# Performance work log

Hardware: AMD Instinct MI355X
Metric: run time of the kernel (lower is better)

Reference implementation:

```python
import jax, jax.numpy as jnp
import numpy as np

N = 50000      # nodes
E = 800000     # edges (avg degree 16)
D = 128        # in_dim
H = 128        # hidden_dim
C = 10         # num_classes
G = 128        # graphs in batch
NUM_LAYERS = 3


def setup_inputs() -> dict:
    key = jax.random.key(0)
    ks = jax.random.split(key, 32)
    inp = {
        'features': jax.random.normal(ks[0], (N, D), dtype=jnp.float32),
        'src': jax.random.randint(ks[1], (E,), 0, N, dtype=jnp.int32),
        'dst': jax.random.randint(ks[2], (E,), 0, N, dtype=jnp.int32),
        'graph_ids': jnp.sort(jax.random.randint(ks[3], (N,), 0, G, dtype=jnp.int32)),
        'eps': jnp.zeros((NUM_LAYERS,), dtype=jnp.float32),  # learn_eps=True, init 0
    }
    # GIN MLPs: layer i has linear1 [in,H], linear2 [H,H] (stored as [in,out])
    ki = 4
    for i in range(NUM_LAYERS):
        din = D if i == 0 else H
        inp[f'w1_{i}'] = jax.random.normal(ks[ki], (din, H), dtype=jnp.float32) * (1.0 / np.sqrt(din)); ki += 1
        inp[f'b1_{i}'] = jnp.zeros((H,), dtype=jnp.float32)
        inp[f'w2_{i}'] = jax.random.normal(ks[ki], (H, H), dtype=jnp.float32) * (1.0 / np.sqrt(H)); ki += 1
        inp[f'b2_{i}'] = jnp.zeros((H,), dtype=jnp.float32)
    inp['wc1'] = jax.random.normal(ks[ki], (H, H), dtype=jnp.float32) * (1.0 / np.sqrt(H)); ki += 1
    inp['bc1'] = jnp.zeros((H,), dtype=jnp.float32)
    inp['wc2'] = jax.random.normal(ks[ki], (H, C), dtype=jnp.float32) * (1.0 / np.sqrt(H)); ki += 1
    inp['bc2'] = jnp.zeros((C,), dtype=jnp.float32)
    return inp


def _mlp(x, w1, b1, w2, b2):
    return jax.nn.relu(x @ w1 + b1) @ w2 + b2


def reference(features, src, dst, graph_ids, eps,
              w1_0, b1_0, w2_0, b2_0,
              w1_1, b1_1, w2_1, b2_1,
              w1_2, b1_2, w2_2, b2_2,
              wc1, bc1, wc2, bc2):
    mlps = [(w1_0, b1_0, w2_0, b2_0), (w1_1, b1_1, w2_1, b2_1), (w1_2, b1_2, w2_2, b2_2)]
    h = features
    for i, (w1, b1, w2, b2) in enumerate(mlps):
        # GINConv: aggregate sum of in-neighbor features (gather src, segment-sum into dst)
        agg = jax.ops.segment_sum(h[src], dst, num_segments=N)
        h = (1.0 + eps[i]) * h + agg
        h = _mlp(h, w1, b1, w2, b2)
        h = jax.nn.relu(h)
    # SumPooling: nodes -> graphs
    hg = jax.ops.segment_sum(h, graph_ids, num_segments=G)  # [G, H]
    out = jax.nn.relu(hg @ wc1 + bc1) @ wc2 + bc2            # [G, C]
    return out
```

## Files before the change

kernel.cpp:

```cpp
#include <hip/hip_runtime.h>

#define NN 50000
#define EE 800000
#define HH 128
#define CC 10
#define GG 128
#define NBK 782
#define NCH 98
#define CHUNK 8192

typedef __attribute__((ext_vector_type(8))) short short8;
typedef __attribute__((ext_vector_type(4))) float f32x4;

__device__ __forceinline__ ushort f2b(float f) {
    union { float f; uint u; } x; x.f = f;
    uint u = x.u;
    uint r = (u + 0x7fffu + ((u >> 16) & 1u)) >> 16;
    return (ushort)r;
}
__device__ __forceinline__ float lo2f(uint v) {
    union { uint u; float f; } x; x.u = v << 16; return x.f;
}
__device__ __forceinline__ float hi2f(uint v) {
    union { uint u; float f; } x; x.u = v & 0xffff0000u; return x.f;
}


__global__ __launch_bounds__(256) void prep_kernel(const float* __restrict__ features,
                                                   const float* w0, const float* w1,
                                                   const float* w2, const float* w3,
                                                   const float* w4, const float* w5,
                                                   const int* __restrict__ dst,
                                                   ushort* __restrict__ hb0,
                                                   ushort* __restrict__ wt,
                                                   int* __restrict__ hist,
                                                   float* __restrict__ hg,
                                                   int* __restrict__ counter) {
    __shared__ int hc[NBK];
    const int b = blockIdx.x, t = threadIdx.x;
    if (b < 6250) {
        int idx = b * 256 + t;
        float4 v = *(const float4*)(features + (size_t)idx * 4);
        ushort4 o;
        o.x = f2b(v.x); o.y = f2b(v.y); o.z = f2b(v.z); o.w = f2b(v.w);
        *(ushort4*)(hb0 + (size_t)idx * 4) = o;
    } else if (b < 6634) {
        int idx = (b - 6250) * 256 + t;
        int mi = idx >> 14, rest = idx & 16383;
        int n = rest >> 7, k = rest & 127;
        const float* src;
        switch (mi) {
            case 0: src = w0; break; case 1: src = w1; break;
            case 2: src = w2; break; case 3: src = w3; break;
            case 4: src = w4; break; default: src = w5; break;
        }
        wt[mi * 16384 + n * 128 + k] = f2b(src[k * 128 + n]);
    } else if (b < 6732) {
        const int c = b - 6634;
        for (int k = t; k < NBK; k += 256) hc[k] = 0;
        __syncthreads();
        for (int j = 0; j < 32; ++j) {
            int e = c * CHUNK + j * 256 + t;
            if (e < EE) atomicAdd(&hc[dst[e] >> 6], 1);
        }
        __syncthreads();
        for (int k = t; k < NBK; k += 256) hist[k * NCH + c] = hc[k];
    } else {
        int idx = (b - 6732) * 256 + t;
        hg[idx] = 0.f;
        if (b == 6732 && t == 0) *counter = 0;
    }
}

__global__ __launch_bounds__(128) void bscan_kernel(const int* __restrict__ hist,
                                                    int* __restrict__ rel,
                                                    int* __restrict__ btot,
                                                    int* __restrict__ bucketbase,
                                                    int* __restrict__ counter) {
    __shared__ int s[128];
    const int b = blockIdx.x, t = threadIdx.x;
    int v = (t < NCH) ? hist[b * NCH + t] : 0;
    s[t] = v;
    __syncthreads();
    for (int off = 1; off < 128; off <<= 1) {
        int tt = (t >= off) ? s[t - off] : 0;
        __syncthreads();
        s[t] += tt;
        __syncthreads();
    }
    if (t < NCH) rel[b * NCH + t] = s[t] - v;
    if (t == 127) {
        btot[b] = s[127];
        bucketbase[b] = atomicAdd(counter, s[127]);
    }
}

__global__ __launch_bounds__(256) void scatter_kernel(const int* __restrict__ src,
                                                      const int* __restrict__ dst,
                                                      const int* __restrict__ rel,
                                                      const int* __restrict__ bucketbase,
                                                      int* __restrict__ epk) {
    __shared__ int cur[NBK];
    const int c = blockIdx.x, t = threadIdx.x;
    for (int k = t; k < NBK; k += 256) cur[k] = bucketbase[k] + rel[k * NCH + c];
    __syncthreads();
    for (int j = 0; j < 32; ++j) {
        int e = c * CHUNK + j * 256 + t;
        if (e < EE) {
            int d = dst[e];
            int bk = d >> 6;
            int pos = atomicAdd(&cur[bk], 1);
            epk[pos] = ((d & 63) << 16) | src[e];
        }
    }
}

__global__ __launch_bounds__(256) void bsort_kernel(const int* __restrict__ epk,
                                                    const int* __restrict__ bucketbase,
                                                    const int* __restrict__ btot,
                                                    ushort* __restrict__ eidx,
                                                    int* __restrict__ rowbeg,
                                                    int* __restrict__ rowend) {
    __shared__ int cnt[64];
    __shared__ int cur[64];
    const int b = blockIdx.x, t = threadIdx.x;
    const int base = bucketbase[b], end = base + btot[b];
    if (t < 64) cnt[t] = 0;
    __syncthreads();
    for (int i = base + t; i < end; i += 256)
        atomicAdd(&cnt[(epk[i] >> 16) & 63], 1);
    __syncthreads();
    if (t < 64) {
        int v = cnt[t];
        int incl = v;
#pragma unroll
        for (int off = 1; off < 64; off <<= 1) {
            int u = __shfl_up(incl, off);
            if (t >= off) incl += u;
        }
        int excl = incl - v;
        cur[t] = excl;
        int node = b * 64 + t;
        if (node < NN) {
            rowbeg[node] = base + excl;
            rowend[node] = base + incl;
        }
    }
    __syncthreads();
    for (int i = base + t; i < end; i += 256) {
        int p = epk[i];
        int dl = (p >> 16) & 63;
        int pos = atomicAdd(&cur[dl], 1);
        eidx[base + pos] = (ushort)(p & 0xffff);
    }
}


__global__ __launch_bounds__(256) void aggregate_kernel(const ushort* __restrict__ h,
                                                        const int* __restrict__ rowbeg,
                                                        const int* __restrict__ rowend,
                                                        const ushort* __restrict__ eidx,
                                                        const float* __restrict__ epsp,
                                                        int layer,
                                                        ushort* __restrict__ xb) {
    const int node = blockIdx.x * 8 + (threadIdx.x >> 5);
    if (node >= NN) return;
    const int li = threadIdx.x & 31;
    const int beg = rowbeg[node], end = rowend[node];
    float c0 = 0.f, c1 = 0.f, c2 = 0.f, c3 = 0.f;
    int i = beg;
    for (; i + 8 <= end; i += 8) {
        int s[8];
        uint2 v[8];
#pragma unroll
        for (int k = 0; k < 8; ++k) s[k] = eidx[i + k];
#pragma unroll
        for (int k = 0; k < 8; ++k)
            v[k] = *(const uint2*)(h + (size_t)s[k] * HH + li * 4);
#pragma unroll
        for (int k = 0; k < 8; ++k) {
            c0 += lo2f(v[k].x); c1 += hi2f(v[k].x);
            c2 += lo2f(v[k].y); c3 += hi2f(v[k].y);
        }
    }
    if (i < end) {
        int s[8];
        uint2 v[8];
#pragma unroll
        for (int k = 0; k < 8; ++k) {
            int idx = i + k;
            s[k] = eidx[idx < end ? idx : end - 1];
        }
#pragma unroll
        for (int k = 0; k < 8; ++k)
            v[k] = *(const uint2*)(h + (size_t)s[k] * HH + li * 4);
#pragma unroll
        for (int k = 0; k < 8; ++k) {
            if (i + k < end) {
                c0 += lo2f(v[k].x); c1 += hi2f(v[k].x);
                c2 += lo2f(v[k].y); c3 += hi2f(v[k].y);
            }
        }
    }
    uint2 hv = *(const uint2*)(h + (size_t)node * HH + li * 4);
    const float e = 1.0f + epsp[layer];
    ushort4 o;
    o.x = f2b(e * lo2f(hv.x) + c0);
    o.y = f2b(e * hi2f(hv.x) + c1);
    o.z = f2b(e * lo2f(hv.y) + c2);
    o.w = f2b(e * hi2f(hv.y) + c3);
    *(ushort4*)(xb + (size_t)node * HH + li * 4) = o;
}


template <bool LAST>
__global__ __launch_bounds__(512) void fused_mlp(const ushort* __restrict__ xb,
                                                 const ushort* __restrict__ wt1,
                                                 const ushort* __restrict__ wt2,
                                                 const float* __restrict__ b1,
                                                 const float* __restrict__ b2,
                                                 const int* __restrict__ gid,
                                                 float* __restrict__ hg,
                                                 ushort* __restrict__ out, int nrows) {
    __shared__ __align__(16) ushort xs[2][64][136];
    __shared__ __align__(16) ushort hs[2][64][136];
    const int tid = threadIdx.x;
    const int lane = tid & 63;
    const int w = (tid >> 6) & 3;
    const int g = tid >> 8;
    const int row0 = blockIdx.x * 128 + g * 64;
    const int l15 = lane & 15, lhi = lane >> 4;
    const int gt = tid & 255;
    const int sr = gt >> 4, skq = gt & 15;

#pragma unroll
    for (int it = 0; it < 4; ++it) {
        int r = it * 16 + sr;
        int row = row0 + r;
        uint4 xv = make_uint4(0u, 0u, 0u, 0u);
        if (row < nrows) xv = *(const uint4*)(xb + (size_t)row * HH + skq * 8);
        *(uint4*)&xs[g][r][skq * 8] = xv;
    }

    short8 a1[2][4], a2[2][4];
#pragma unroll
    for (int fa = 0; fa < 2; ++fa)
#pragma unroll
        for (int kt = 0; kt < 4; ++kt) {
            int n = w * 32 + fa * 16 + l15;
            int k = kt * 32 + lhi * 8;
            a1[fa][kt] = *(const short8*)(wt1 + n * HH + k);
            a2[fa][kt] = *(const short8*)(wt2 + n * HH + k);
        }
    __syncthreads();

    f32x4 acc[2][4];
#pragma unroll
    for (int fa = 0; fa < 2; ++fa)
#pragma unroll
        for (int fb = 0; fb < 4; ++fb) acc[fa][fb] = (f32x4)(0.f);
#pragma unroll
    for (int kt = 0; kt < 4; ++kt) {
        short8 bfr[4];
#pragma unroll
        for (int fb = 0; fb < 4; ++fb)
            bfr[fb] = *(const short8*)&xs[g][fb * 16 + l15][kt * 32 + lhi * 8];
#pragma unroll
        for (int fa = 0; fa < 2; ++fa)
#pragma unroll
            for (int fb = 0; fb < 4; ++fb)
                acc[fa][fb] = __builtin_amdgcn_mfma_f32_16x16x32_bf16(a1[fa][kt], bfr[fb],
                                                                     acc[fa][fb], 0, 0, 0);
    }

#pragma unroll
    for (int fa = 0; fa < 2; ++fa) {
        int nb = w * 32 + fa * 16 + lhi * 4;
        float4 bv = *(const float4*)(b1 + nb);
#pragma unroll
        for (int fb = 0; fb < 4; ++fb) {
            ushort4 o;
            o.x = f2b(fmaxf(acc[fa][fb][0] + bv.x, 0.f));
            o.y = f2b(fmaxf(acc[fa][fb][1] + bv.y, 0.f));
            o.z = f2b(fmaxf(acc[fa][fb][2] + bv.z, 0.f));
            o.w = f2b(fmaxf(acc[fa][fb][3] + bv.w, 0.f));
            *(ushort4*)&hs[g][fb * 16 + l15][nb] = o;
        }
    }
    __syncthreads();

#pragma unroll
    for (int fa = 0; fa < 2; ++fa)
#pragma unroll
        for (int fb = 0; fb < 4; ++fb) acc[fa][fb] = (f32x4)(0.f);
#pragma unroll
    for (int kt = 0; kt < 4; ++kt) {
        short8 bfr[4];
#pragma unroll
        for (int fb = 0; fb < 4; ++fb)
            bfr[fb] = *(const short8*)&hs[g][fb * 16 + l15][kt * 32 + lhi * 8];
#pragma unroll
        for (int fa = 0; fa < 2; ++fa)
#pragma unroll
            for (int fb = 0; fb < 4; ++fb)
                acc[fa][fb] = __builtin_amdgcn_mfma_f32_16x16x32_bf16(a2[fa][kt], bfr[fb],
                                                                     acc[fa][fb], 0, 0, 0);
    }

#pragma unroll
    for (int fa = 0; fa < 2; ++fa) {
        int nb = w * 32 + fa * 16 + lhi * 4;
        float4 bv = *(const float4*)(b2 + nb);
#pragma unroll
        for (int fb = 0; fb < 4; ++fb) {
            int m = row0 + fb * 16 + l15;
            ushort4 o;
            o.x = f2b(fmaxf(acc[fa][fb][0] + bv.x, 0.f));
            o.y = f2b(fmaxf(acc[fa][fb][1] + bv.y, 0.f));
            o.z = f2b(fmaxf(acc[fa][fb][2] + bv.z, 0.f));
            o.w = f2b(fmaxf(acc[fa][fb][3] + bv.w, 0.f));
            if (LAST) {
                *(ushort4*)&xs[g][fb * 16 + l15][nb] = o;
            } else if (m < nrows) {
                *(ushort4*)(out + (size_t)m * HH + nb) = o;
            }
        }
    }

    if (LAST) {
        __syncthreads();
        int j = gt & 63;
        int rg = gt >> 6;
        float ax = 0.f, ay = 0.f;
        int gcur = -1;
#pragma unroll
        for (int ii = 0; ii < 16; ++ii) {
            int r = rg + ii * 4;
            int n = row0 + r;
            if (n >= nrows) break;
            int gv = gid[n];
            if (gv != gcur) {
                if (gcur >= 0) {
                    atomicAdd(&hg[gcur * HH + 2 * j], ax);
                    atomicAdd(&hg[gcur * HH + 2 * j + 1], ay);
                }
                gcur = gv; ax = 0.f; ay = 0.f;
            }
            uint v = *(const uint*)&xs[g][r][2 * j];
            ax += lo2f(v); ay += hi2f(v);
        }
        if (gcur >= 0) {
            atomicAdd(&hg[gcur * HH + 2 * j], ax);
            atomicAdd(&hg[gcur * HH + 2 * j + 1], ay);
        }
    }
}


__global__ __launch_bounds__(128) void classify_kernel(const float* __restrict__ hg,
                                                       const float* __restrict__ wc1,
                                                       const float* __restrict__ bc1,
                                                       const float* __restrict__ wc2,
                                                       const float* __restrict__ bc2,
                                                       float* __restrict__ out) {
    __shared__ float xrow[HH];
    __shared__ float trow[HH];
    int g = blockIdx.x, j = threadIdx.x;
    xrow[j] = hg[g * HH + j];
    __syncthreads();
    float s = bc1[j];
#pragma unroll 8
    for (int k = 0; k < HH; ++k) s += xrow[k] * wc1[k * HH + j];
    trow[j] = fmaxf(s, 0.f);
    __syncthreads();
    if (j < CC) {
        float o = bc2[j];
#pragma unroll 8
        for (int k = 0; k < HH; ++k) o += trow[k] * wc2[k * CC + j];
        out[g * CC + j] = o;
    }
}

extern "C" void kernel_launch(void* const* d_in, const int* in_sizes, int n_in,
                              void* d_out, int out_size, void* d_ws, size_t ws_size,
                              hipStream_t stream) {
    const float* features = (const float*)d_in[0];
    const int* src = (const int*)d_in[1];
    const int* dst = (const int*)d_in[2];
    const int* gid = (const int*)d_in[3];
    const float* eps = (const float*)d_in[4];
    const float* w1[3] = {(const float*)d_in[5], (const float*)d_in[9], (const float*)d_in[13]};
    const float* b1[3] = {(const float*)d_in[6], (const float*)d_in[10], (const float*)d_in[14]};
    const float* w2[3] = {(const float*)d_in[7], (const float*)d_in[11], (const float*)d_in[15]};
    const float* b2[3] = {(const float*)d_in[8], (const float*)d_in[12], (const float*)d_in[16]};
    const float* wc1 = (const float*)d_in[17];
    const float* bc1 = (const float*)d_in[18];
    const float* wc2 = (const float*)d_in[19];
    const float* bc2 = (const float*)d_in[20];
    float* outp = (float*)d_out;

    char* ws = (char*)d_ws;
    size_t off = 0;
    auto alloc = [&](size_t bytes) {
        void* p = ws + off;
        off += (bytes + 255) & ~(size_t)255;
        return p;
    };
    int* hist = (int*)alloc((size_t)NBK * NCH * sizeof(int));
    int* rel = (int*)alloc((size_t)NBK * NCH * sizeof(int));
    int* btot = (int*)alloc(NBK * sizeof(int));
    int* bucketbase = (int*)alloc(NBK * sizeof(int));
    int* counter = (int*)alloc(256);
    int* epk = (int*)alloc(EE * sizeof(int));
    ushort* eidx = (ushort*)alloc(EE * sizeof(ushort));
    int* rowbeg = (int*)alloc(NN * sizeof(int));
    int* rowend = (int*)alloc(NN * sizeof(int));
    ushort* hb0 = (ushort*)alloc((size_t)NN * HH * 2);
    ushort* hbuf = (ushort*)alloc((size_t)NN * HH * 2);
    ushort* xb = (ushort*)alloc((size_t)NN * HH * 2);
    ushort* wtb = (ushort*)alloc(6 * 16384 * 2);
    float* hg = (float*)alloc(GG * HH * sizeof(float));

    prep_kernel<<<6796, 256, 0, stream>>>(features, w1[0], w2[0], w1[1], w2[1], w1[2], w2[2],
                                          dst, hb0, wtb, hist, hg, counter);
    bscan_kernel<<<NBK, 128, 0, stream>>>(hist, rel, btot, bucketbase, counter);
    scatter_kernel<<<NCH, 256, 0, stream>>>(src, dst, rel, bucketbase, epk);
    bsort_kernel<<<NBK, 256, 0, stream>>>(epk, bucketbase, btot, eidx, rowbeg, rowend);

    const int GB = (NN + 127) / 128;
    const int AB = (NN + 7) / 8;

    aggregate_kernel<<<AB, 256, 0, stream>>>(hb0, rowbeg, rowend, eidx, eps, 0, xb);
    fused_mlp<false><<<GB, 512, 0, stream>>>(xb, wtb + 0 * 16384, wtb + 1 * 16384,
                                             b1[0], b2[0], gid, hg, hbuf, NN);
    aggregate_kernel<<<AB, 256, 0, stream>>>(hbuf, rowbeg, rowend, eidx, eps, 1, xb);
    fused_mlp<false><<<GB, 512, 0, stream>>>(xb, wtb + 2 * 16384, wtb + 3 * 16384,
                                             b1[1], b2[1], gid, hg, hbuf, NN);
    aggregate_kernel<<<AB, 256, 0, stream>>>(hbuf, rowbeg, rowend, eidx, eps, 2, xb);
    fused_mlp<true><<<GB, 512, 0, stream>>>(xb, wtb + 4 * 16384, wtb + 5 * 16384,
                                            b1[2], b2[2], gid, hg, nullptr, NN);

    classify_kernel<<<GG, 128, 0, stream>>>(hg, wc1, bc1, wc2, bc2, outp);
}
```

Before: 213.9 us.

## Halve fused MLP block threads, process two row tiles sequentially with prefetch

The fused MLP kernel now uses 256 threads per block instead of two independent 512-thread groups. Each block processes its two 64-row tiles in sequence and prefetches the second tile into registers while the first is computed. The hidden LDS buffer shrinks to a single tile, and the weight fragments loaded into registers are reused across both tiles. The cost is less parallelism per block and tile work that is no longer concurrent, which may expose latency if occupancy does not make up for it.

```diff
diff --git a/kernel.cpp b/kernel.cpp
--- a/kernel.cpp
+++ b/kernel.cpp
@@ -214,7 +214,7 @@
 
 
 template <bool LAST>
-__global__ __launch_bounds__(512) void fused_mlp(const ushort* __restrict__ xb,
+__global__ __launch_bounds__(256) void fused_mlp(const ushort* __restrict__ xb,
                                                  const ushort* __restrict__ wt1,
                                                  const ushort* __restrict__ wt2,
                                                  const float* __restrict__ b1,
@@ -223,23 +223,20 @@
                                                  float* __restrict__ hg,
                                                  ushort* __restrict__ out, int nrows) {
     __shared__ __align__(16) ushort xs[2][64][136];
-    __shared__ __align__(16) ushort hs[2][64][136];
+    __shared__ __align__(16) ushort hs[64][136];
     const int tid = threadIdx.x;
-    const int lane = tid & 63;
-    const int w = (tid >> 6) & 3;
-    const int g = tid >> 8;
-    const int row0 = blockIdx.x * 128 + g * 64;
+    const int lane = tid & 63, w = tid >> 6;
+    const int row0 = blockIdx.x * 128;
     const int l15 = lane & 15, lhi = lane >> 4;
-    const int gt = tid & 255;
-    const int sr = gt >> 4, skq = gt & 15;
-
+    const int sr = tid >> 4, skq = tid & 15;
+
+    uint4 st[4];
 #pragma unroll
     for (int it = 0; it < 4; ++it) {
         int r = it * 16 + sr;
         int row = row0 + r;
-        uint4 xv = make_uint4(0u, 0u, 0u, 0u);
-        if (row < nrows) xv = *(const uint4*)(xb + (size_t)row * HH + skq * 8);
-        *(uint4*)&xs[g][r][skq * 8] = xv;
+        st[it] = make_uint4(0u, 0u, 0u, 0u);
+        if (row < nrows) st[it] = *(const uint4*)(xb + (size_t)row * HH + skq * 8);
     }
 
     short8 a1[2][4], a2[2][4];
@@ -252,106 +249,121 @@
             a1[fa][kt] = *(const short8*)(wt1 + n * HH + k);
             a2[fa][kt] = *(const short8*)(wt2 + n * HH + k);
         }
-    __syncthreads();
+
+#pragma unroll
+    for (int it = 0; it < 4; ++it) *(uint4*)&xs[0][it * 16 + sr][skq * 8] = st[it];
+    __syncthreads();
+
+#pragma unroll
+    for (int it = 0; it < 4; ++it) {
+        int r = it * 16 + sr;
+        int row = row0 + 64 + r;
+        st[it] = make_uint4(0u, 0u, 0u, 0u);
+        if (row < nrows) st[it] = *(const uint4*)(xb + (size_t)row * HH + skq * 8);
+    }
 
     f32x4 acc[2][4];
 #pragma unroll
-    for (int fa = 0; fa < 2; ++fa)
-#pragma unroll
-        for (int fb = 0; fb < 4; ++fb) acc[fa][fb] = (f32x4)(0.f);
-#pragma unroll
-    for (int kt = 0; kt < 4; ++kt) {
-        short8 bfr[4];
-#pragma unroll
-        for (int fb = 0; fb < 4; ++fb)
-            bfr[fb] = *(const short8*)&xs[g][fb * 16 + l15][kt * 32 + lhi * 8];
+    for (int tile = 0; tile < 2; ++tile) {
+        const int rt0 = row0 + tile * 64;
 #pragma unroll
         for (int fa = 0; fa < 2; ++fa)
 #pragma unroll
+            for (int fb = 0; fb < 4; ++fb) acc[fa][fb] = (f32x4)(0.f);
+#pragma unroll
+        for (int kt = 0; kt < 4; ++kt) {
+            short8 bfr[4];
+#pragma unroll
             for (int fb = 0; fb < 4; ++fb)
-                acc[fa][fb] = __builtin_amdgcn_mfma_f32_16x16x32_bf16(a1[fa][kt], bfr[fb],
-                                                                     acc[fa][fb], 0, 0, 0);
-    }
-
-#pragma unroll
-    for (int fa = 0; fa < 2; ++fa) {
-        int nb = w * 32 + fa * 16 + lhi * 4;
-        float4 bv = *(const float4*)(b1 + nb);
-#pragma unroll
-        for (int fb = 0; fb < 4; ++fb) {
-            ushort4 o;
-            o.x = f2b(fmaxf(acc[fa][fb][0] + bv.x, 0.f));
-            o.y = f2b(fmaxf(acc[fa][fb][1] + bv.y, 0.f));
-            o.z = f2b(fmaxf(acc[fa][fb][2] + bv.z, 0.f));
-            o.w = f2b(fmaxf(acc[fa][fb][3] + bv.w, 0.f));
-            *(ushort4*)&hs[g][fb * 16 + l15][nb] = o;
-        }
-    }
-    __syncthreads();
-
-#pragma unroll
-    for (int fa = 0; fa < 2; ++fa)
-#pragma unroll
-        for (int fb = 0; fb < 4; ++fb) acc[fa][fb] = (f32x4)(0.f);
-#pragma unroll
-    for (int kt = 0; kt < 4; ++kt) {
-        short8 bfr[4];
-#pragma unroll
-        for (int fb = 0; fb < 4; ++fb)
-            bfr[fb] = *(const short8*)&hs[g][fb * 16 + l15][kt * 32 + lhi * 8];
+                bfr[fb] = *(const short8*)&xs[tile][fb * 16 + l15][kt * 32 + lhi * 8];
+#pragma unroll
+            for (int fa = 0; fa < 2; ++fa)
+#pragma unroll
+                for (int fb = 0; fb < 4; ++fb)
+                    acc[fa][fb] = __builtin_amdgcn_mfma_f32_16x16x32_bf16(a1[fa][kt], bfr[fb],
+                                                                         acc[fa][fb], 0, 0, 0);
+        }
+#pragma unroll
+        for (int fa = 0; fa < 2; ++fa) {
+            int nb = w * 32 + fa * 16 + lhi * 4;
+            float4 bv = *(const float4*)(b1 + nb);
+#pragma unroll
+            for (int fb = 0; fb < 4; ++fb) {
+                ushort4 o;
+                o.x = f2b(fmaxf(acc[fa][fb][0] + bv.x, 0.f));
+                o.y = f2b(fmaxf(acc[fa][fb][1] + bv.y, 0.f));
+                o.z = f2b(fmaxf(acc[fa][fb][2] + bv.z, 0.f));
+                o.w = f2b(fmaxf(acc[fa][fb][3] + bv.w, 0.f));
+                *(ushort4*)&hs[fb * 16 + l15][nb] = o;
+            }
+        }
+        __syncthreads();
 #pragma unroll
         for (int fa = 0; fa < 2; ++fa)
 #pragma unroll
+            for (int fb = 0; fb < 4; ++fb) acc[fa][fb] = (f32x4)(0.f);
+#pragma unroll
+        for (int kt = 0; kt < 4; ++kt) {
+            short8 bfr[4];
+#pragma unroll
             for (int fb = 0; fb < 4; ++fb)
-                acc[fa][fb] = __builtin_amdgcn_mfma_f32_16x16x32_bf16(a2[fa][kt], bfr[fb],
-                                                                     acc[fa][fb], 0, 0, 0);
-    }
-
-#pragma unroll
-    for (int fa = 0; fa < 2; ++fa) {
-        int nb = w * 32 + fa * 16 + lhi * 4;
-        float4 bv = *(const float4*)(b2 + nb);
-#pragma unroll
-        for (int fb = 0; fb < 4; ++fb) {
-            int m = row0 + fb * 16 + l15;
-            ushort4 o;
-            o.x = f2b(fmaxf(acc[fa][fb][0] + bv.x, 0.f));
-            o.y = f2b(fmaxf(acc[fa][fb][1] + bv.y, 0.f));
-            o.z = f2b(fmaxf(acc[fa][fb][2] + bv.z, 0.f));
-            o.w = f2b(fmaxf(acc[fa][fb][3] + bv.w, 0.f));
-            if (LAST) {
-                *(ushort4*)&xs[g][fb * 16 + l15][nb] = o;
-            } else if (m < nrows) {
-                *(ushort4*)(out + (size_t)m * HH + nb) = o;
+                bfr[fb] = *(const short8*)&hs[fb * 16 + l15][kt * 32 + lhi * 8];
+#pragma unroll
+            for (int fa = 0; fa < 2; ++fa)
+#pragma unroll
+                for (int fb = 0; fb < 4; ++fb)
+                    acc[fa][fb] = __builtin_amdgcn_mfma_f32_16x16x32_bf16(a2[fa][kt], bfr[fb],
+                                                                         acc[fa][fb], 0, 0, 0);
+        }
+#pragma unroll
+        for (int fa = 0; fa < 2; ++fa) {
+            int nb = w * 32 + fa * 16 + lhi * 4;
+            float4 bv = *(const float4*)(b2 + nb);
+#pragma unroll
+            for (int fb = 0; fb < 4; ++fb) {
+                int m = rt0 + fb * 16 + l15;
+                ushort4 o;
+                o.x = f2b(fmaxf(acc[fa][fb][0] + bv.x, 0.f));
+                o.y = f2b(fmaxf(acc[fa][fb][1] + bv.y, 0.f));
+                o.z = f2b(fmaxf(acc[fa][fb][2] + bv.z, 0.f));
+                o.w = f2b(fmaxf(acc[fa][fb][3] + bv.w, 0.f));
+                if (LAST) {
+                    *(ushort4*)&xs[tile][fb * 16 + l15][nb] = o;
+                } else if (m < nrows) {
+                    *(ushort4*)(out + (size_t)m * HH + nb) = o;
+                }
             }
         }
-    }
-
-    if (LAST) {
-        __syncthreads();
-        int j = gt & 63;
-        int rg = gt >> 6;
-        float ax = 0.f, ay = 0.f;
-        int gcur = -1;
-#pragma unroll
-        for (int ii = 0; ii < 16; ++ii) {
-            int r = rg + ii * 4;
-            int n = row0 + r;
-            if (n >= nrows) break;
-            int gv = gid[n];
-            if (gv != gcur) {
-                if (gcur >= 0) {
-                    atomicAdd(&hg[gcur * HH + 2 * j], ax);
-                    atomicAdd(&hg[gcur * HH + 2 * j + 1], ay);
+        if (tile == 0) {
+#pragma unroll
+            for (int it = 0; it < 4; ++it) *(uint4*)&xs[1][it * 16 + sr][skq * 8] = st[it];
+        }
+        __syncthreads();
+        if (LAST) {
+            int j = tid & 63;
+            int rg = tid >> 6;
+            float ax = 0.f, ay = 0.f;
+            int gcur = -1;
+#pragma unroll
+            for (int ii = 0; ii < 16; ++ii) {
+                int r = rg + ii * 4;
+                int n = rt0 + r;
+                if (n >= nrows) break;
+                int g = gid[n];
+                if (g != gcur) {
+                    if (gcur >= 0) {
+                        atomicAdd(&hg[gcur * HH + 2 * j], ax);
+                        atomicAdd(&hg[gcur * HH + 2 * j + 1], ay);
+                    }
+                    gcur = g; ax = 0.f; ay = 0.f;
                 }
-                gcur = gv; ax = 0.f; ay = 0.f;
+                uint v = *(const uint*)&xs[tile][r][2 * j];
+                ax += lo2f(v); ay += hi2f(v);
             }
-            uint v = *(const uint*)&xs[g][r][2 * j];
-            ax += lo2f(v); ay += hi2f(v);
-        }
-        if (gcur >= 0) {
-            atomicAdd(&hg[gcur * HH + 2 * j], ax);
-            atomicAdd(&hg[gcur * HH + 2 * j + 1], ay);
+            if (gcur >= 0) {
+                atomicAdd(&hg[gcur * HH + 2 * j], ax);
+                atomicAdd(&hg[gcur * HH + 2 * j + 1], ay);
+            }
         }
     }
 }
@@ -431,13 +443,13 @@
     const int AB = (NN + 7) / 8;
 
     aggregate_kernel<<<AB, 256, 0, stream>>>(hb0, rowbeg, rowend, eidx, eps, 0, xb);
-    fused_mlp<false><<<GB, 512, 0, stream>>>(xb, wtb + 0 * 16384, wtb + 1 * 16384,
+    fused_mlp<false><<<GB, 256, 0, stream>>>(xb, wtb + 0 * 16384, wtb + 1 * 16384,
                                              b1[0], b2[0], gid, hg, hbuf, NN);
     aggregate_kernel<<<AB, 256, 0, stream>>>(hbuf, rowbeg, rowend, eidx, eps, 1, xb);
-    fused_mlp<false><<<GB, 512, 0, stream>>>(xb, wtb + 2 * 16384, wtb + 3 * 16384,
+    fused_mlp<false><<<GB, 256, 0, stream>>>(xb, wtb + 2 * 16384, wtb + 3 * 16384,
                                              b1[1], b2[1], gid, hg, hbuf, NN);
     aggregate_kernel<<<AB, 256, 0, stream>>>(hbuf, rowbeg, rowend, eidx, eps, 2, xb);
-    fused_mlp<true><<<GB, 512, 0, stream>>>(xb, wtb + 4 * 16384, wtb + 5 * 16384,
+    fused_mlp<true><<<GB, 256, 0, stream>>>(xb, wtb + 4 * 16384, wtb + 5 * 16384,
                                             b1[2], b2[2], gid, hg, nullptr, NN);
 
     classify_kernel<<<GG, 128, 0, stream>>>(hg, wc1, bc1, wc2, bc2, outp);
```

Result: no change. 213.6 us (-0.2%).
